# Performance work log

Hardware: AMD Instinct MI355X
Metric: run time of the kernel (lower is better)

Reference implementation:

```python
import jax, jax.numpy as jnp
import numpy as np

DIM = 512
HEADS = 8
DIM_HEAD = 64
NUM_MEM_KV = 4
H = W = 128


def setup_inputs() -> dict:
    key = jax.random.key(0)
    k1, k2, k3, k4 = jax.random.split(key, 4)
    return {
        "x": jax.random.normal(k1, (DIM, H, W), dtype=jnp.float32),
        "norm1_gamma": jnp.zeros((DIM, 1, 1), dtype=jnp.float32),
        "qkv_w": jax.random.normal(k2, (3 * HEADS * DIM_HEAD, DIM), dtype=jnp.float32) * (DIM ** -0.5),
        "mem_kv": jax.random.normal(k3, (2, HEADS, DIM_HEAD, NUM_MEM_KV), dtype=jnp.float32),
        "conv_w": jax.random.normal(k4, (DIM, HEADS * DIM_HEAD), dtype=jnp.float32) * ((HEADS * DIM_HEAD) ** -0.5),
        "conv_b": jnp.zeros((DIM,), dtype=jnp.float32),
        "norm2_gamma": jnp.zeros((DIM, 1, 1), dtype=jnp.float32),
    }


def rms_norm(x, gamma, dim):
    # x: (c, h, w); L2 norm over channel axis, rescale by sqrt(dim)*(gamma+1)
    n = jnp.linalg.norm(x, ord=2, axis=0)  # (h, w)
    return x / n * (gamma + 1.0) * (dim ** 0.5)


def reference(x, norm1_gamma, qkv_w, mem_kv, conv_w, conv_b, norm2_gamma):
    c, h, w = x.shape
    scale = DIM_HEAD ** -0.5
    xn = rms_norm(x, norm1_gamma, DIM)
    # 1x1 conv == channel matmul
    qkv = jnp.einsum('oc,cxy->oxy', qkv_w, xn)  # (3*hidden, h, w)
    q, k, v = jnp.split(qkv, 3, axis=0)
    def to_heads(t):
        return t.reshape(HEADS, DIM_HEAD, h * w)  # (H, d, n)
    q, k, v = to_heads(q), to_heads(k), to_heads(v)
    mk, mv = mem_kv[0], mem_kv[1]  # (H, d, m)
    k = jnp.concatenate([mk, k], axis=-1)
    v = jnp.concatenate([mv, v], axis=-1)
    q = jax.nn.softmax(q, axis=-2) * scale  # softmax over feature dim d
    k = jax.nn.softmax(k, axis=-1)          # softmax over sequence dim n
    context = jnp.einsum('hdn,hen->hde', k, v)  # (H, d, e)
    out = jnp.einsum('hde,hdn->hen', context, q)  # (H, e, n)
    out = out.reshape(HEADS * DIM_HEAD, h, w)
    out = jnp.einsum('oc,cxy->oxy', conv_w, out) + conv_b[:, None, None]
    return rms_norm(out, norm2_gamma, DIM)
```

## Files before the change

kernel.cpp:

```cpp
#include <hip/hip_runtime.h>
#include <hip/hip_bf16.h>
#include <cstdint>


typedef unsigned short u16;
typedef unsigned int   u32;
typedef short bf16x8 __attribute__((ext_vector_type(8)));
typedef float f32x4  __attribute__((ext_vector_type(4)));

#define HW    16384
#define CDIM  512
#define SQRTD 22.627416997969522f

#define WAITV8 asm volatile("s_waitcnt vmcnt(8)" ::: "memory")
#define WAITV0 asm volatile("s_waitcnt vmcnt(0)" ::: "memory")
#define WAITL0 asm volatile("s_waitcnt lgkmcnt(0)" ::: "memory")

__device__ __forceinline__ u16 f2bf(float f) {
  u32 x = __builtin_bit_cast(u32, f);
  u32 r = x + 0x7fffu + ((x >> 16) & 1u);
  return (u16)(r >> 16);
}

__device__ __forceinline__ void gload16(const void* g, void* l) {
  __builtin_amdgcn_global_load_lds(
      (const __attribute__((address_space(1))) void*)(uintptr_t)g,
      (__attribute__((address_space(3))) void*)(u32)(uintptr_t)l,
      16, 0, 0);
}

__global__ __launch_bounds__(512) void k_pre(const float* __restrict__ x, const float* __restrict__ g1,
                                             const float* __restrict__ qkvw, const float* __restrict__ memkv,
                                             u16* __restrict__ xnt, u16* __restrict__ wbf,
                                             float* __restrict__ den, float* __restrict__ ctx16) {
  __shared__ float tl[512 * 68];
  __shared__ float ssp[8][64];
  __shared__ float rs[64];
  __shared__ float gl[512];
  int t = threadIdx.x, l = t & 63, w = t >> 6;
  int b = blockIdx.x;
  int p0 = b * 64;
  #pragma unroll
  for (int i = 0; i < 16; i++) {
    int idx = i * 512 + t;
    int c = idx >> 4, p4 = (idx & 15) * 4;
    float4 v = *(const float4*)(x + (size_t)c * HW + p0 + p4);
    *(float4*)&tl[c * 68 + p4] = v;
  }
  if (t < 512) gl[t] = 1.0f + g1[t];
  {
    float4 z = make_float4(0.f, 0.f, 0.f, 0.f);
    *(float4*)(ctx16 + (size_t)b * 2048 + t * 4) = z;
  }
  __syncthreads();
  {
    float s = 0.f;
    #pragma unroll
    for (int c = 0; c < 64; c++) {
      float v = tl[(w * 64 + c) * 68 + l];
      s += v * v;
    }
    ssp[w][l] = s;
  }
  __syncthreads();
  if (t < 64) {
    float s = 0.f;
    #pragma unroll
    for (int j = 0; j < 8; j++) s += ssp[j][t];
    rs[t] = SQRTD * rsqrtf(s);
  }
  __syncthreads();
  #pragma unroll
  for (int i = 0; i < 8; i++) {
    int c0 = (i * 8 + w) * 8;
    float sp = rs[l];
    u32 pk[4];
    #pragma unroll
    for (int j = 0; j < 4; j++) {
      float a = tl[(c0 + 2 * j) * 68 + l] * sp * gl[c0 + 2 * j];
      float bq = tl[(c0 + 2 * j + 1) * 68 + l] * sp * gl[c0 + 2 * j + 1];
      pk[j] = (u32)f2bf(a) | ((u32)f2bf(bq) << 16);
    }
    *(uint4*)&xnt[(size_t)(p0 + l) * CDIM + c0] = make_uint4(pk[0], pk[1], pk[2], pk[3]);
  }
  #pragma unroll
  for (int sweep = 0; sweep < 2; sweep++) {
    int idx = (sweep * 256 * 512 + b * 512 + t) * 4;
    if (idx < 1536 * 512) {
      float4 v = *(const float4*)(qkvw + idx);
      ushort4 o; o.x = f2bf(v.x); o.y = f2bf(v.y); o.z = f2bf(v.z); o.w = f2bf(v.w);
      *(ushort4*)(wbf + idx) = o;
    }
  }
  if (b == 0 && t < 512) {
    int h = t >> 6, d = t & 63;
    const float* mk = memkv + ((size_t)h * 64 + d) * 4;
    den[t] = __expf(mk[0]) + __expf(mk[1]) + __expf(mk[2]) + __expf(mk[3]);
  }
}

__global__ __launch_bounds__(256, 2) void k_gemm1(const u16* __restrict__ A, const u16* __restrict__ Bt,
                                                  u16* __restrict__ qT, float* __restrict__ den,
                                                  float* __restrict__ ctx16) {
  const int K = CDIM;
  __shared__ u16 As[2][128 * 64], Bs[2][128 * 64];
  __shared__ float dred[2][64];
  int t = threadIdx.x;
  int lane = t & 63, w = t >> 6;
  int lq = lane >> 4, lr = lane & 15;
  int wg = blockIdx.x;
  int gt = (wg & 7) * 192 + (wg >> 3);
  int bn = gt / 12, bm = gt % 12;
  int wm = (w >> 1) * 64, wn = (w & 1) * 64;
  int h = bm - 4;
  int rb01 = (bm < 4) ? bm * 128 : 512 + h * 64;
  int rb23 = (bm < 4) ? bm * 128 : 960 + h * 64;
  f32x4 acc[4][4] = {};
  const u16* Bbase = Bt + (size_t)bn * 128 * K;

  auto STAGE = [&](int buf, int kt) {
    #pragma unroll
    for (int i = 0; i < 4; i++) {
      int s = i * 256 + t;
      int row = s >> 3, slot = (s & 7) ^ (row & 7);
      int rb = (i < 2) ? rb01 : rb23;
      gload16(A + (size_t)(rb + row) * K + kt * 64 + slot * 8, &As[buf][(i * 256 + (w << 6)) * 8]);
    }
    #pragma unroll
    for (int i = 0; i < 4; i++) {
      int s = i * 256 + t;
      int row = s >> 3, slot = (s & 7) ^ (row & 7);
      gload16(Bbase + (size_t)row * K + kt * 64 + slot * 8, &Bs[buf][(i * 256 + (w << 6)) * 8]);
    }
  };
  auto FRAGS = [&](int buf, int kk, bf16x8* af, bf16x8* bv) {
    #pragma unroll
    for (int mi = 0; mi < 4; mi++) {
      int row = wm + mi * 16 + lr;
      int slot = ((kk << 2) + lq) ^ (row & 7);
      af[mi] = *(const bf16x8*)&As[buf][row * 64 + slot * 8];
    }
    #pragma unroll
    for (int nj = 0; nj < 4; nj++) {
      int row = wn + nj * 16 + lr;
      int slot = ((kk << 2) + lq) ^ (row & 7);
      bv[nj] = *(const bf16x8*)&Bs[buf][row * 64 + slot * 8];
    }
  };

  STAGE(0, 0);
  STAGE(1, 1);
  for (int kt = 0; kt < 7; kt++) {
    int buf = kt & 1;
    WAITV8;
    __builtin_amdgcn_s_barrier();
    bf16x8 af0[4], bv0[4], af1[4], bv1[4];
    FRAGS(buf, 0, af0, bv0);
    FRAGS(buf, 1, af1, bv1);
    WAITL0;
    __builtin_amdgcn_s_barrier();
    if (kt < 6) STAGE(buf, kt + 2);
    __builtin_amdgcn_s_setprio(1);
    #pragma unroll
    for (int mi = 0; mi < 4; mi++)
      #pragma unroll
      for (int nj = 0; nj < 4; nj++)
        acc[mi][nj] = __builtin_amdgcn_mfma_f32_16x16x32_bf16(af0[mi], bv0[nj], acc[mi][nj], 0, 0, 0);
    #pragma unroll
    for (int mi = 0; mi < 4; mi++)
      #pragma unroll
      for (int nj = 0; nj < 4; nj++)
        acc[mi][nj] = __builtin_amdgcn_mfma_f32_16x16x32_bf16(af1[mi], bv1[nj], acc[mi][nj], 0, 0, 0);
    __builtin_amdgcn_s_setprio(0);
  }
  {
    WAITV0;
    __builtin_amdgcn_s_barrier();
    bf16x8 af0[4], bv0[4], af1[4], bv1[4];
    FRAGS(1, 0, af0, bv0);
    FRAGS(1, 1, af1, bv1);
    __builtin_amdgcn_s_setprio(1);
    #pragma unroll
    for (int mi = 0; mi < 4; mi++)
      #pragma unroll
      for (int nj = 0; nj < 4; nj++)
        acc[mi][nj] = __builtin_amdgcn_mfma_f32_16x16x32_bf16(af0[mi], bv0[nj], acc[mi][nj], 0, 0, 0);
    #pragma unroll
    for (int mi = 0; mi < 4; mi++)
      #pragma unroll
      for (int nj = 0; nj < 4; nj++)
        acc[mi][nj] = __builtin_amdgcn_mfma_f32_16x16x32_bf16(af1[mi], bv1[nj], acc[mi][nj], 0, 0, 0);
    __builtin_amdgcn_s_setprio(0);
  }

  if (bm < 4) {
    int cm0 = bm * 128 + wm, cn0 = bn * 128 + wn;
    #pragma unroll
    for (int nj = 0; nj < 4; nj++) {
      float e[4][4];
      float s = 0.f;
      #pragma unroll
      for (int mi = 0; mi < 4; mi++)
        #pragma unroll
        for (int r = 0; r < 4; r++) { e[mi][r] = __expf(acc[mi][nj][r]); s += e[mi][r]; }
      s += __shfl_xor(s, 16);
      s += __shfl_xor(s, 32);
      float inv = 1.0f / s;
      int col = cn0 + nj * 16 + lr;
      #pragma unroll
      for (int mi = 0; mi < 4; mi++) {
        ushort4 o;
        o.x = f2bf(e[mi][0] * inv); o.y = f2bf(e[mi][1] * inv);
        o.z = f2bf(e[mi][2] * inv); o.w = f2bf(e[mi][3] * inv);
        *(ushort4*)&qT[(size_t)col * CDIM + cm0 + mi * 16 + lq * 4] = o;
      }
    }
  } else {
    __syncthreads();
    u16* Ks = &As[0][0];
    u16* Vs = &Bs[0][0];
    if (w < 2) {
      #pragma unroll
      for (int mi = 0; mi < 4; mi++)
        #pragma unroll
        for (int r = 0; r < 4; r++) {
          int d = mi * 16 + lq * 4 + r;
          float rsum = 0.f;
          #pragma unroll
          for (int nj = 0; nj < 4; nj++) {
            float e = __expf(acc[mi][nj][r]);
            rsum += e;
            int px = wn + nj * 16 + lr;
            Ks[d * 128 + (((px >> 3) ^ (d & 7)) << 3) + (px & 7)] = f2bf(e);
          }
          rsum += __shfl_xor(rsum, 1); rsum += __shfl_xor(rsum, 2);
          rsum += __shfl_xor(rsum, 4); rsum += __shfl_xor(rsum, 8);
          if (lr == 0) dred[w][d] = rsum;
        }
    } else {
      #pragma unroll
      for (int mi = 0; mi < 4; mi++)
        #pragma unroll
        for (int r = 0; r < 4; r++) {
          int e = mi * 16 + lq * 4 + r;
          #pragma unroll
          for (int nj = 0; nj < 4; nj++) {
            int px = wn + nj * 16 + lr;
            Vs[e * 128 + (((px >> 3) ^ (e & 7)) << 3) + (px & 7)] = f2bf(acc[mi][nj][r]);
          }
        }
    }
    __syncthreads();
    if (t < 64) atomicAdd(&den[h * 64 + t], dred[0][t] + dred[1][t]);
    f32x4 c2[4] = {};
    #pragma unroll
    for (int ks = 0; ks < 4; ks++) {
      int ra = w * 16 + lr;
      bf16x8 a = *(const bf16x8*)&Ks[ra * 128 + (((ks * 4 + lq) ^ (ra & 7)) << 3)];
      #pragma unroll
      for (int nj = 0; nj < 4; nj++) {
        int rb2 = nj * 16 + lr;
        bf16x8 b = *(const bf16x8*)&Vs[rb2 * 128 + (((ks * 4 + lq) ^ (rb2 & 7)) << 3)];
        c2[nj] = __builtin_amdgcn_mfma_f32_16x16x32_bf16(a, b, c2[nj], 0, 0, 0);
      }
    }
    float* cp = ctx16 + ((size_t)(bn & 15) * 8 + h) * 4096;
    #pragma unroll
    for (int nj = 0; nj < 4; nj++)
      #pragma unroll
      for (int r = 0; r < 4; r++) {
        int d = w * 16 + lq * 4 + r, e = nj * 16 + lr;
        atomicAdd(&cp[d * 64 + e], c2[nj][r]);
      }
  }
}

__global__ __launch_bounds__(256) void k_fold(const float* __restrict__ convw, const float* __restrict__ ctx16,
                                              const float* __restrict__ den, const float* __restrict__ memkv,
                                              u16* __restrict__ Mbf) {
  __shared__ float cn[64 * 65];
  __shared__ float dn[64];
  __shared__ float emk[256];
  __shared__ float smv[256];
  int t = threadIdx.x;
  int h = blockIdx.x & 7, oc = blockIdx.x >> 3;
  if (t < 64) dn[t] = 0.125f / den[h * 64 + t];
  if (t < 256) emk[t] = __expf(memkv[(size_t)h * 256 + t]);
  if (t < 256) smv[t] = memkv[(size_t)(512 * 4) + h * 256 + t];
  __syncthreads();
  #pragma unroll
  for (int i = 0; i < 16; i++) {
    int idx = i * 256 + t;
    int d = idx >> 6, e = idx & 63;
    float s = emk[d * 4] * smv[e * 4] + emk[d * 4 + 1] * smv[e * 4 + 1]
            + emk[d * 4 + 2] * smv[e * 4 + 2] + emk[d * 4 + 3] * smv[e * 4 + 3];
    #pragma unroll
    for (int rep = 0; rep < 16; rep++) s += ctx16[((size_t)rep * 8 + h) * 4096 + idx];
    cn[d * 65 + e] = s * dn[d];
  }
  __syncthreads();
  int o = oc * 64 + (t >> 2);
  int d0 = (t & 3) * 16;
  float Wr[64];
  const float* wp = convw + (size_t)o * CDIM + h * 64;
  #pragma unroll
  for (int e4 = 0; e4 < 16; e4++) {
    float4 v = *(const float4*)(wp + e4 * 4);
    Wr[e4 * 4] = v.x; Wr[e4 * 4 + 1] = v.y; Wr[e4 * 4 + 2] = v.z; Wr[e4 * 4 + 3] = v.w;
  }
  float outv[16];
  #pragma unroll
  for (int dd = 0; dd < 16; dd++) {
    float a = 0.f;
    #pragma unroll
    for (int e = 0; e < 64; e++) a += Wr[e] * cn[(d0 + dd) * 65 + e];
    outv[dd] = a;
  }
  #pragma unroll
  for (int j = 0; j < 8; j++) {
    u32 v = (u32)f2bf(outv[j * 2]) | ((u32)f2bf(outv[j * 2 + 1]) << 16);
    *(u32*)&Mbf[(size_t)o * CDIM + h * 64 + d0 + j * 2] = v;
  }
}

__global__ __launch_bounds__(512) void k_gemm2(const u16* __restrict__ A, const u16* __restrict__ Bt,
                                               const float* __restrict__ bias, const float* __restrict__ g2,
                                               float* __restrict__ out) {
  __shared__ u16 As[512 * 64];
  __shared__ u16 Bs[64 * 64];
  __shared__ float css[64];
  int t = threadIdx.x; int lane = t & 63, w = t >> 6, lq = lane >> 4, lr = lane & 15;
  int bn = blockIdx.x;
  if (t < 64) css[t] = 0.f;
  const u16* Bbase = Bt + (size_t)bn * 64 * CDIM;
  f32x4 acc[4][4] = {};
  for (int kt = 0; kt < 8; kt++) {
    #pragma unroll
    for (int i = 0; i < 8; i++) {
      int s = i * 512 + t;
      int row = s >> 3, slot = (s & 7) ^ (row & 7);
      gload16(A + (size_t)row * CDIM + kt * 64 + slot * 8, &As[(i * 512 + (w << 6)) * 8]);
    }
    {
      int row = t >> 3, slot = (t & 7) ^ (row & 7);
      gload16(Bbase + (size_t)row * CDIM + kt * 64 + slot * 8, &Bs[(w << 6) * 8]);
    }
    __syncthreads();
    #pragma unroll
    for (int kk = 0; kk < 2; kk++) {
      bf16x8 af[4], bv[4];
      #pragma unroll
      for (int mi = 0; mi < 4; mi++) {
        int row = w * 64 + mi * 16 + lr;
        int slot = ((kk << 2) + lq) ^ (row & 7);
        af[mi] = *(const bf16x8*)&As[row * 64 + slot * 8];
      }
      #pragma unroll
      for (int nj = 0; nj < 4; nj++) {
        int row = nj * 16 + lr;
        int slot = ((kk << 2) + lq) ^ (row & 7);
        bv[nj] = *(const bf16x8*)&Bs[row * 64 + slot * 8];
      }
      __builtin_amdgcn_s_setprio(1);
      #pragma unroll
      for (int mi = 0; mi < 4; mi++)
        #pragma unroll
        for (int nj = 0; nj < 4; nj++)
          acc[mi][nj] = __builtin_amdgcn_mfma_f32_16x16x32_bf16(af[mi], bv[nj], acc[mi][nj], 0, 0, 0);
      __builtin_amdgcn_s_setprio(0);
    }
    __syncthreads();
  }
  float bb[4][4];
  float ps[4] = {0.f, 0.f, 0.f, 0.f};
  #pragma unroll
  for (int mi = 0; mi < 4; mi++)
    #pragma unroll
    for (int r = 0; r < 4; r++) {
      int rowg = w * 64 + mi * 16 + lq * 4 + r;
      bb[mi][r] = bias[rowg];
      #pragma unroll
      for (int nj = 0; nj < 4; nj++) {
        float v = acc[mi][nj][r] + bb[mi][r];
        ps[nj] += v * v;
      }
    }
  #pragma unroll
  for (int nj = 0; nj < 4; nj++) {
    ps[nj] += __shfl_xor(ps[nj], 16);
    ps[nj] += __shfl_xor(ps[nj], 32);
  }
  if (lq == 0) {
    #pragma unroll
    for (int nj = 0; nj < 4; nj++) atomicAdd(&css[nj * 16 + lr], ps[nj]);
  }
  __syncthreads();
  float sc[4];
  #pragma unroll
  for (int nj = 0; nj < 4; nj++) sc[nj] = SQRTD * rsqrtf(css[nj * 16 + lr]);
  #pragma unroll
  for (int mi = 0; mi < 4; mi++)
    #pragma unroll
    for (int r = 0; r < 4; r++) {
      int rowg = w * 64 + mi * 16 + lq * 4 + r;
      float g = 1.0f + g2[rowg];
      #pragma unroll
      for (int nj = 0; nj < 4; nj++) {
        float v = acc[mi][nj][r] + bb[mi][r];
        out[(size_t)rowg * HW + bn * 64 + nj * 16 + lr] = v * sc[nj] * g;
      }
    }
}

extern "C" void kernel_launch(void* const* d_in, const int* in_sizes, int n_in,
                              void* d_out, int out_size, void* d_ws, size_t ws_size,
                              hipStream_t stream) {
  (void)in_sizes; (void)n_in; (void)out_size; (void)ws_size;
  const float* x     = (const float*)d_in[0];
  const float* g1    = (const float*)d_in[1];
  const float* qkvw  = (const float*)d_in[2];
  const float* memkv = (const float*)d_in[3];
  const float* convw = (const float*)d_in[4];
  const float* convb = (const float*)d_in[5];
  const float* g2    = (const float*)d_in[6];
  float* out = (float*)d_out;
  char* ws = (char*)d_ws;

  float* den   = (float*)(ws);
  float* ctx16 = (float*)(ws + 4096);
  u16* Mbf     = (u16*)(ws + 2101248);
  u16* wbf     = (u16*)(ws + 2625536);
  u16* xnt     = (u16*)(ws + 4198400);
  u16* qT      = (u16*)(ws + 20975616);

  k_pre<<<256, 512, 0, stream>>>(x, g1, qkvw, memkv, xnt, wbf, den, ctx16);
  k_gemm1<<<1536, 256, 0, stream>>>(wbf, xnt, qT, den, ctx16);
  k_fold<<<64, 256, 0, stream>>>(convw, ctx16, den, memkv, Mbf);
  k_gemm2<<<256, 512, 0, stream>>>(Mbf, qT, convb, g2, out);
}
```

Measured before the change: 92.31 us.

## Restructure QKV GEMM main loop into interleaved half-step A/B staging

Measured after the change: 94.98 us. 1.03x slower.

```diff
diff --git a/kernel.cpp b/kernel.cpp
--- a/kernel.cpp
+++ b/kernel.cpp
@@ -12,9 +12,9 @@
 #define CDIM  512
 #define SQRTD 22.627416997969522f
 
-#define WAITV8 asm volatile("s_waitcnt vmcnt(8)" ::: "memory")
 #define WAITV0 asm volatile("s_waitcnt vmcnt(0)" ::: "memory")
 #define WAITL0 asm volatile("s_waitcnt lgkmcnt(0)" ::: "memory")
+#define SCHED0 __builtin_amdgcn_sched_barrier(0)
 
 __device__ __forceinline__ u16 f2bf(float f) {
   u32 x = __builtin_bit_cast(u32, f);
@@ -118,7 +118,7 @@
   f32x4 acc[4][4] = {};
   const u16* Bbase = Bt + (size_t)bn * 128 * K;
 
-  auto STAGE = [&](int buf, int kt) {
+  auto STAGE_A = [&](int buf, int kt) {
     #pragma unroll
     for (int i = 0; i < 4; i++) {
       int s = i * 256 + t;
@@ -126,6 +126,8 @@
       int rb = (i < 2) ? rb01 : rb23;
       gload16(A + (size_t)(rb + row) * K + kt * 64 + slot * 8, &As[buf][(i * 256 + (w << 6)) * 8]);
     }
+  };
+  auto STAGE_B = [&](int buf, int kt) {
     #pragma unroll
     for (int i = 0; i < 4; i++) {
       int s = i * 256 + t;
@@ -148,49 +150,41 @@
     }
   };
 
-  STAGE(0, 0);
-  STAGE(1, 1);
-  for (int kt = 0; kt < 7; kt++) {
+  STAGE_A(0, 0);
+  STAGE_B(0, 0);
+  WAITV0;
+  __builtin_amdgcn_s_barrier();
+  SCHED0;
+  for (int kt = 0; kt < 8; kt++) {
     int buf = kt & 1;
-    WAITV8;
-    __builtin_amdgcn_s_barrier();
     bf16x8 af0[4], bv0[4], af1[4], bv1[4];
     FRAGS(buf, 0, af0, bv0);
-    FRAGS(buf, 1, af1, bv1);
+    if (kt < 7) STAGE_A(buf ^ 1, kt + 1);
     WAITL0;
-    __builtin_amdgcn_s_barrier();
-    if (kt < 6) STAGE(buf, kt + 2);
+    SCHED0;
     __builtin_amdgcn_s_setprio(1);
     #pragma unroll
     for (int mi = 0; mi < 4; mi++)
       #pragma unroll
       for (int nj = 0; nj < 4; nj++)
         acc[mi][nj] = __builtin_amdgcn_mfma_f32_16x16x32_bf16(af0[mi], bv0[nj], acc[mi][nj], 0, 0, 0);
+    __builtin_amdgcn_s_setprio(0);
+    FRAGS(buf, 1, af1, bv1);
+    if (kt < 7) STAGE_B(buf ^ 1, kt + 1);
+    WAITL0;
+    SCHED0;
+    __builtin_amdgcn_s_setprio(1);
     #pragma unroll
     for (int mi = 0; mi < 4; mi++)
       #pragma unroll
       for (int nj = 0; nj < 4; nj++)
         acc[mi][nj] = __builtin_amdgcn_mfma_f32_16x16x32_bf16(af1[mi], bv1[nj], acc[mi][nj], 0, 0, 0);
     __builtin_amdgcn_s_setprio(0);
-  }
-  {
-    WAITV0;
-    __builtin_amdgcn_s_barrier();
-    bf16x8 af0[4], bv0[4], af1[4], bv1[4];
-    FRAGS(1, 0, af0, bv0);
-    FRAGS(1, 1, af1, bv1);
-    __builtin_amdgcn_s_setprio(1);
-    #pragma unroll
-    for (int mi = 0; mi < 4; mi++)
-      #pragma unroll
-      for (int nj = 0; nj < 4; nj++)
-        acc[mi][nj] = __builtin_amdgcn_mfma_f32_16x16x32_bf16(af0[mi], bv0[nj], acc[mi][nj], 0, 0, 0);
-    #pragma unroll
-    for (int mi = 0; mi < 4; mi++)
-      #pragma unroll
-      for (int nj = 0; nj < 4; nj++)
-        acc[mi][nj] = __builtin_amdgcn_mfma_f32_16x16x32_bf16(af1[mi], bv1[nj], acc[mi][nj], 0, 0, 0);
-    __builtin_amdgcn_s_setprio(0);
+    if (kt < 7) {
+      WAITV0;
+      __builtin_amdgcn_s_barrier();
+      SCHED0;
+    }
   }
 
   if (bm < 4) {
```
